# Optimization experiments

Measured on AMD Instinct MI355X. Metric: run time of the kernel, lower is better.

## Reference

```python
import jax, jax.numpy as jnp
import numpy as np
import math

B, L, D, K = 4, 2048, 1024, 3
PAD = K // 2
EPS_LN = 1e-5
EPS_NORM = 1e-12


def dwsep_conv(x_bld, dw, dwb, pw, pwb):
    # x_bld: [B, L, D] -> depthwise conv over L (groups=D) then pointwise 1x1
    x = jnp.transpose(x_bld, (0, 2, 1))  # [B, D, L]
    y = jax.lax.conv_general_dilated(
        x, dw, window_strides=(1,), padding=[(PAD, PAD)],
        feature_group_count=D, dimension_numbers=("NCH", "OIH", "NCH"))
    y = y + dwb[None, :, None]
    y = jnp.einsum("bcl,oc->bol", y, pw) + pwb[None, :, None]
    return jnp.transpose(y, (0, 2, 1))  # [B, L, D]


def l2norm(x):
    n = jnp.sqrt(jnp.sum(x * x, axis=-1, keepdims=True))
    return x / jnp.maximum(n, EPS_NORM)


def layernorm(x, g, b):
    mu = jnp.mean(x, axis=-1, keepdims=True)
    var = jnp.mean((x - mu) ** 2, axis=-1, keepdims=True)
    return (x - mu) * jax.lax.rsqrt(var + EPS_LN) * g + b


def setup_inputs() -> dict:
    key = jax.random.key(0)
    ks = jax.random.split(key, 24)
    s = 0.02
    def w(k, shape, scale=s):
        return (jax.random.normal(k, shape, dtype=jnp.float32) * scale)
    inp = {
        "x": jax.random.normal(ks[0], (B, L, D), dtype=jnp.float32),
        "wq": w(ks[1], (D, D)), "bq": jnp.zeros((D,), jnp.float32),
        "wk": w(ks[2], (D, D)), "bk": jnp.zeros((D,), jnp.float32),
        "wv": w(ks[3], (D, D)), "bv": jnp.zeros((D,), jnp.float32),
        "dwq": w(ks[4], (D, 1, K), 0.1), "dwq_b": jnp.zeros((D,), jnp.float32),
        "pwq": w(ks[5], (D, D)), "pwq_b": jnp.zeros((D,), jnp.float32),
        "dwk": w(ks[6], (D, 1, K), 0.1), "dwk_b": jnp.zeros((D,), jnp.float32),
        "pwk": w(ks[7], (D, D)), "pwk_b": jnp.zeros((D,), jnp.float32),
        "dwv": w(ks[8], (D, 1, K), 0.1), "dwv_b": jnp.zeros((D,), jnp.float32),
        "pwv": w(ks[9], (D, D)), "pwv_b": jnp.zeros((D,), jnp.float32),
        "wg": w(ks[10], (D, D)), "bg": jnp.zeros((D,), jnp.float32),
        "wo": w(ks[11], (D, D)), "bo": jnp.zeros((D,), jnp.float32),
        "mem_w": w(ks[12], (D, D)),
        "ln_g": jnp.ones((D,), jnp.float32),
        "ln_b": jnp.zeros((D,), jnp.float32),
    }
    return inp


def reference(x, wq, bq, wk, bk, wv, bv,
              dwq, dwq_b, pwq, pwq_b,
              dwk, dwk_b, pwk, pwk_b,
              dwv, dwv_b, pwv, pwv_b,
              wg, bg, wo, bo, mem_w, ln_g, ln_b):
    residual = x
    Q = jax.nn.silu(jnp.einsum("bld,ed->ble", x, wq) + bq)
    Kt = jax.nn.silu(jnp.einsum("bld,ed->ble", x, wk) + bk)
    V = jax.nn.silu(jnp.einsum("bld,ed->ble", x, wv) + bv)
    Q = dwsep_conv(Q, dwq, dwq_b, pwq, pwq_b)
    Kt = dwsep_conv(Kt, dwk, dwk_b, pwk, pwk_b)
    V = dwsep_conv(V, dwv, dwv_b, pwv, pwv_b)
    Qn = l2norm(Q)
    Kn = l2norm(Kt)
    scores = jnp.einsum("bqd,bkd->bqk", Qn, Kn) / math.sqrt(D)
    attn = jax.nn.softmax(scores, axis=-1)
    attn_out = jnp.einsum("bqk,bkd->bqd", attn, V)
    gate = jax.nn.sigmoid(jnp.einsum("bld,ed->ble", attn_out, wg) + bg)
    gated = gate * attn_out
    out = jnp.einsum("bld,ed->ble", gated, wo) + bo + residual
    out = layernorm(out, ln_g, ln_b)
    mem_pred = jnp.einsum("bld,de->ble", Kn, mem_w)
    mem_loss = jnp.mean((mem_pred - V) ** 2)
    return (out, mem_loss)
```

## Files before the change

kernel.cpp:

```cpp
#include <hip/hip_runtime.h>
#include <stdint.h>

typedef __attribute__((ext_vector_type(8))) short short8;
typedef __attribute__((ext_vector_type(4))) short short4v;
typedef __attribute__((ext_vector_type(4))) float f32x4;

#define DEV static __device__ __forceinline__

static constexpr int LL = 2048;
static constexpr int DD = 1024;
static constexpr long long BLD = 8388608LL;
static constexpr long long SLD = 2097152LL;
static constexpr long long SLLB = 4194304LL;

DEV short f2bf(float f) {
    uint32_t u = __builtin_bit_cast(uint32_t, f);
    u += 0x7fffu + ((u >> 16) & 1u);
    return (short)(u >> 16);
}
DEV float bf2f(short s) {
    uint32_t u = ((uint32_t)(uint16_t)s) << 16;
    return __builtin_bit_cast(float, u);
}

DEV float waveSum(float v) {
#pragma unroll
    for (int o = 32; o; o >>= 1) v += __shfl_down(v, o);
    return v;
}

DEV void gload16(const void* g, void* l) {
    __builtin_amdgcn_global_load_lds(
        (const __attribute__((address_space(1))) uint32_t*)(uintptr_t)g,
        (__attribute__((address_space(3))) uint32_t*)(uintptr_t)l,
        16, 0, 0);
}

__global__ __launch_bounds__(256) void k_prep(
    const float* __restrict__ x,
    const float* wq, const float* wk, const float* wv,
    const float* pq, const float* pk, const float* pv,
    const float* wg, const float* wo,
    const float* bq, const float* bk, const float* bv,
    const float* pqb, const float* pkb, const float* pvb,
    const float* __restrict__ memw,
    short* Wqkv, short* Pqkv, short* Wg, short* Wo,
    float* bqkv, float* bpw, short* MwT, short* xb, float* loss) {
    __shared__ float tile[64][65];
    const int bid = blockIdx.x;
    const int t = threadIdx.x;

    if (bid < 4096) {
        const int w = bid >> 9;
        const long long i = (long long)((bid & 511) * 256 + t) * 8;
        const float* src; short* dst;
        switch (w) {
            case 0: src = wq; dst = Wqkv;                break;
            case 1: src = wk; dst = Wqkv + 1048576;      break;
            case 2: src = wv; dst = Wqkv + 2097152;      break;
            case 3: src = pq; dst = Pqkv;                break;
            case 4: src = pk; dst = Pqkv + 1048576;      break;
            case 5: src = pv; dst = Pqkv + 2097152;      break;
            case 6: src = wg; dst = Wg;                  break;
            default: src = wo; dst = Wo;                 break;
        }
        const float4* p = (const float4*)(src + i);
        float4 a = p[0], b = p[1];
        short8 o;
        o[0] = f2bf(a.x); o[1] = f2bf(a.y); o[2] = f2bf(a.z); o[3] = f2bf(a.w);
        o[4] = f2bf(b.x); o[5] = f2bf(b.y); o[6] = f2bf(b.z); o[7] = f2bf(b.w);
        *(short8*)(dst + i) = o;
    } else if (bid < 4120) {
        const int idx = (bid - 4096) * 256 + t;
        const int sel = idx >> 10, j = idx & 1023;
        const float* s;
        switch (sel) {
            case 0: s = bq; break; case 1: s = bk; break; case 2: s = bv; break;
            case 3: s = pqb; break; case 4: s = pkb; break; default: s = pvb; break;
        }
        float v = s[j];
        if (sel < 3) bqkv[sel * 1024 + j] = v;
        else         bpw[(sel - 3) * 1024 + j] = v;
    } else if (bid < 4376) {
        const int tt = bid - 4120;
        const int r0 = (tt >> 4) * 64, c0 = (tt & 15) * 64;
#pragma unroll
        for (int i = 0; i < 16; i++) {
            int lin = i * 256 + t; int lr = lin >> 6, lc = lin & 63;
            tile[lr][lc] = memw[(long long)(r0 + lr) * DD + (c0 + lc)];
        }
        __syncthreads();
#pragma unroll
        for (int i = 0; i < 16; i++) {
            int lin = i * 256 + t; int orr = lin >> 6, oc = lin & 63;
            MwT[(long long)(c0 + orr) * DD + (r0 + oc)] = f2bf(tile[oc][orr]);
        }
    } else if (bid < 8472) {
        const long long i = (long long)((bid - 4376) * 256 + t) * 8;
        const float4* p = (const float4*)(x + i);
        float4 a = p[0], b = p[1];
        short8 o;
        o[0] = f2bf(a.x); o[1] = f2bf(a.y); o[2] = f2bf(a.z); o[3] = f2bf(a.w);
        o[4] = f2bf(b.x); o[5] = f2bf(b.y); o[6] = f2bf(b.z); o[7] = f2bf(b.w);
        *(short8*)(xb + i) = o;
    } else {
        if (t == 0) *loss = 0.f;
    }
}

__global__ __launch_bounds__(256) void k_dwconv3b(const short* __restrict__ in,
                                                  const float* __restrict__ dwq,
                                                  const float* __restrict__ dwk,
                                                  const float* __restrict__ dwv,
                                                  const float* __restrict__ dbq,
                                                  const float* __restrict__ dbk,
                                                  const float* __restrict__ dbv,
                                                  short* __restrict__ outp) {
    const int idx = blockIdx.x * 256 + threadIdx.x;
    const int d8 = idx & 127;
    const int lc = (idx >> 7) & 255;
    const int b  = (idx >> 15) & 3;
    const int br = idx >> 17;
    const float* dw = (br == 0) ? dwq : (br == 1) ? dwk : dwv;
    const float* db = (br == 0) ? dbq : (br == 1) ? dbk : dbv;

    float w[24], bb[8];
    {
        const float4* wp = (const float4*)(dw + d8 * 24);
#pragma unroll
        for (int i = 0; i < 6; i++) {
            float4 tt = wp[i];
            w[i * 4 + 0] = tt.x; w[i * 4 + 1] = tt.y;
            w[i * 4 + 2] = tt.z; w[i * 4 + 3] = tt.w;
        }
        const float4* bp = (const float4*)(db + d8 * 8);
        float4 t0 = bp[0], t1 = bp[1];
        bb[0] = t0.x; bb[1] = t0.y; bb[2] = t0.z; bb[3] = t0.w;
        bb[4] = t1.x; bb[5] = t1.y; bb[6] = t1.z; bb[7] = t1.w;
    }

    const int l0 = lc * 8;
    const long long base = ((long long)(b * LL + l0)) * 3072 + br * 1024 + d8 * 8;
    short8 xr[10];
#pragma unroll
    for (int i = 0; i < 10; i++) {
        const int l = l0 - 1 + i;
        if (l >= 0 && l < LL) xr[i] = *(const short8*)(in + base + (long long)(i - 1) * 3072);
        else { short8 z = {0, 0, 0, 0, 0, 0, 0, 0}; xr[i] = z; }
    }
#pragma unroll
    for (int j = 0; j < 8; j++) {
        short8 o;
#pragma unroll
        for (int c = 0; c < 8; c++) {
            float v = bb[c] + w[c * 3 + 0] * bf2f(xr[j][c])
                            + w[c * 3 + 1] * bf2f(xr[j + 1][c])
                            + w[c * 3 + 2] * bf2f(xr[j + 2][c]);
            o[c] = f2bf(v);
        }
        *(short8*)(outp + base + (long long)j * 3072) = o;
    }
}

__global__ __launch_bounds__(256) void k_vt_norm(const short* __restrict__ vb,
                                                 short* __restrict__ VT,
                                                 const short* __restrict__ qkb,
                                                 float* __restrict__ ninv) {
    __shared__ short tile[64][65];
    __shared__ float red[4];
    const int bid = blockIdx.x;
    const int t = threadIdx.x;
    if (bid < 2048) {
        const int z = bid >> 9, tt = bid & 511;
        const int r0 = (tt >> 4) * 64, c0 = (tt & 15) * 64;
        const short* in = vb + (long long)z * SLD;
        short* out = VT + (long long)z * SLD;
#pragma unroll
        for (int i = 0; i < 16; i++) {
            int lin = i * 256 + t; int lr = lin >> 6, lc = lin & 63;
            tile[lr][lc] = in[(long long)(r0 + lr) * 1024 + (c0 + lc)];
        }
        __syncthreads();
#pragma unroll
        for (int i = 0; i < 16; i++) {
            int lin = i * 256 + t; int orr = lin >> 6, oc = lin & 63;
            out[(long long)(c0 + orr) * 2048 + (r0 + oc)] = tile[oc][orr];
        }
    } else {
        const long long row = bid - 2048;
        const short* p = qkb + row * DD;
        short4v v = *(const short4v*)(p + t * 4);
        float f0 = bf2f(v[0]), f1 = bf2f(v[1]), f2 = bf2f(v[2]), f3 = bf2f(v[3]);
        float ss = f0 * f0 + f1 * f1 + f2 * f2 + f3 * f3;
        ss = waveSum(ss);
        if ((t & 63) == 0) red[t >> 6] = ss;
        __syncthreads();
        ss = (red[0] + red[1]) + (red[2] + red[3]);
        if (t == 0) ninv[row] = 1.f / fmaxf(sqrtf(ss), 1e-12f);
    }
}

__global__ __launch_bounds__(256) void k_rowsuminv(const short* __restrict__ sp,
                                                   float* __restrict__ rinv) {
    __shared__ float red[4];
    const long long row = blockIdx.x;
    const short* p = sp + row * 2048;
    const int t = threadIdx.x;
    short8 v = *(short8*)(p + t * 8);
    float s = 0.f;
#pragma unroll
    for (int j = 0; j < 8; j++) s += bf2f(v[j]);
    s = waveSum(s);
    if ((t & 63) == 0) red[t >> 6] = s;
    __syncthreads();
    s = (red[0] + red[1]) + (red[2] + red[3]);
    if (t == 0) rinv[row] = 1.f / s;
}

__global__ __launch_bounds__(256) void k_layernorm(float* __restrict__ y,
                                                   const float* __restrict__ g,
                                                   const float* __restrict__ b) {
    __shared__ float redS[4], redQ[4];
    const long long row = blockIdx.x;
    float* p = y + row * DD;
    const int t = threadIdx.x;
    float4 v = *(float4*)(p + t * 4);
    float s = v.x + v.y + v.z + v.w;
    float q = v.x * v.x + v.y * v.y + v.z * v.z + v.w * v.w;
    s = waveSum(s); q = waveSum(q);
    if ((t & 63) == 0) { redS[t >> 6] = s; redQ[t >> 6] = q; }
    __syncthreads();
    s = (redS[0] + redS[1]) + (redS[2] + redS[3]);
    q = (redQ[0] + redQ[1]) + (redQ[2] + redQ[3]);
    float mu = s * (1.f / DD);
    float var = q * (1.f / DD) - mu * mu;
    float rs = rsqrtf(var + 1e-5f);
    float4 o;
    o.x = (v.x - mu) * rs * g[t * 4 + 0] + b[t * 4 + 0];
    o.y = (v.y - mu) * rs * g[t * 4 + 1] + b[t * 4 + 1];
    o.z = (v.z - mu) * rs * g[t * 4 + 2] + b[t * 4 + 2];
    o.w = (v.w - mu) * rs * g[t * 4 + 3] + b[t * 4 + 3];
    *(float4*)(p + t * 4) = o;
}

enum { EPI_SILU, EPI_BIAS, EPI_EXPS, EPI_GATE, EPI_RESID };

template <int EPI>
__global__ __launch_bounds__(256, 4) void gemm(
    const short* __restrict__ A, int lda, long long sAb,
    const short* __restrict__ W, int ldw, long long sWb,
    void* __restrict__ outv, int ldo, long long sOb,
    const float* __restrict__ bias, long long sBias,
    const void* __restrict__ aux,
    int K, float scale) {
    __shared__ short lds[16384];

    const int z = blockIdx.z;
    A += (long long)z * sAb;
    W += (long long)z * sWb;

    const int tid = threadIdx.x;
    const int wid = tid >> 6, lane = tid & 63;
    const int row0 = blockIdx.y * 128, col0 = blockIdx.x * 128;
    const int wrM = (wid >> 1) * 64, wcN = (wid & 1) * 64;
    const int rl = lane & 15, kcl = lane >> 4;

    f32x4 acc[4][4] = {};

    const int srow = tid >> 3;
    const int cswz = (tid & 7) ^ (srow & 7);
    long long offA[4], offB[4];
#pragma unroll
    for (int j = 0; j < 4; j++) {
        const int rr = j * 32 + srow;
        offA[j] = (long long)(row0 + rr) * lda + cswz * 8;
        offB[j] = (long long)(col0 + rr) * ldw + cswz * 8;
    }

    const int nk = K >> 6;
    const int swz0 = (kcl ^ (rl & 7)) * 8;
    const int swz1 = ((kcl + 4) ^ (rl & 7)) * 8;

    for (int t = 0; t < nk; ++t) {
        const short* a = A + (long long)t * 64;
        const short* w = W + (long long)t * 64;
#pragma unroll
        for (int j = 0; j < 4; j++)
            gload16(a + offA[j], lds + (j * 256 + tid) * 8);
#pragma unroll
        for (int j = 0; j < 4; j++)
            gload16(w + offB[j], lds + 8192 + (j * 256 + tid) * 8);
        asm volatile("s_waitcnt vmcnt(0)" ::: "memory");
        __builtin_amdgcn_s_barrier();

        short8 af[4], bfr[4];
#pragma unroll
        for (int mi = 0; mi < 4; mi++)
            af[mi] = *(const short8*)&lds[(wrM + mi * 16 + rl) * 64 + swz0];
#pragma unroll
        for (int ni = 0; ni < 4; ni++)
            bfr[ni] = *(const short8*)&lds[8192 + (wcN + ni * 16 + rl) * 64 + swz0];
        __builtin_amdgcn_s_setprio(1);
#pragma unroll
        for (int mi = 0; mi < 4; mi++)
#pragma unroll
            for (int ni = 0; ni < 4; ni++)
                acc[mi][ni] = __builtin_amdgcn_mfma_f32_16x16x32_bf16(
                    af[mi], bfr[ni], acc[mi][ni], 0, 0, 0);
        __builtin_amdgcn_s_setprio(0);
#pragma unroll
        for (int mi = 0; mi < 4; mi++)
            af[mi] = *(const short8*)&lds[(wrM + mi * 16 + rl) * 64 + swz1];
#pragma unroll
        for (int ni = 0; ni < 4; ni++)
            bfr[ni] = *(const short8*)&lds[8192 + (wcN + ni * 16 + rl) * 64 + swz1];
        __builtin_amdgcn_s_setprio(1);
#pragma unroll
        for (int mi = 0; mi < 4; mi++)
#pragma unroll
            for (int ni = 0; ni < 4; ni++)
                acc[mi][ni] = __builtin_amdgcn_mfma_f32_16x16x32_bf16(
                    af[mi], bfr[ni], acc[mi][ni], 0, 0, 0);
        __builtin_amdgcn_s_setprio(0);
        __builtin_amdgcn_s_barrier();
    }

    const int lr4 = (lane >> 4) * 4;
    float bcol[4];
    if constexpr (EPI == EPI_SILU || EPI == EPI_BIAS || EPI == EPI_GATE || EPI == EPI_RESID) {
        const float* bz = bias + (long long)z * sBias;
#pragma unroll
        for (int ni = 0; ni < 4; ni++) bcol[ni] = bz[col0 + wcN + ni * 16 + rl];
    }
    if constexpr (EPI == EPI_EXPS) {
        const float* kz = (const float*)aux + (long long)z * 2048;
#pragma unroll
        for (int ni = 0; ni < 4; ni++) bcol[ni] = kz[col0 + wcN + ni * 16 + rl];
    }
    const float* qz = (EPI == EPI_EXPS) ? bias + (long long)z * sBias : nullptr;
#pragma unroll
    for (int mi = 0; mi < 4; mi++) {
#pragma unroll
        for (int ni = 0; ni < 4; ni++) {
            const int gc = col0 + wcN + ni * 16 + rl;
#pragma unroll
            for (int r = 0; r < 4; r++) {
                const int gr = row0 + wrM + mi * 16 + lr4 + r;
                const long long oi = (long long)gr * ldo + gc;
                float v = acc[mi][ni][r];
                if constexpr (EPI == EPI_SILU) {
                    v += bcol[ni];
                    v = v / (1.f + __expf(-v));
                    ((short*)outv + (long long)z * sOb)[oi] = f2bf(v);
                } else if constexpr (EPI == EPI_BIAS) {
                    ((short*)outv + (long long)z * sOb)[oi] = f2bf(v + bcol[ni]);
                } else if constexpr (EPI == EPI_EXPS) {
                    ((short*)outv + (long long)z * sOb)[oi] =
                        f2bf(__expf(v * qz[gr] * bcol[ni] * scale));
                } else if constexpr (EPI == EPI_GATE) {
                    float g = 1.f / (1.f + __expf(-(v + bcol[ni])));
                    float a = bf2f(((const short*)aux)[oi]);
                    ((short*)outv)[oi] = f2bf(g * a);
                } else if constexpr (EPI == EPI_RESID) {
                    ((float*)outv)[oi] = v + bcol[ni] + ((const float*)aux)[oi];
                }
            }
        }
    }
}

__global__ __launch_bounds__(256, 4) void k_avml(
    const short* __restrict__ P, const short* __restrict__ VT,
    const float* __restrict__ rinv, short* __restrict__ aob,
    const short* __restrict__ kb, const short* __restrict__ MwT,
    const short* __restrict__ vb, const float* __restrict__ kinv,
    float* __restrict__ lossOut) {
    __shared__ short lds[16384];

    const int bid = blockIdx.x;
    const bool isAV = bid < 512;
    const short* A; const short* W;
    int lda, ldw, K, row0, col0;
    const float* rp = nullptr;
    short* outp = nullptr;
    if (isAV) {
        const int z = bid >> 7, rem = bid & 127;
        row0 = (rem >> 3) * 128; col0 = (rem & 7) * 128;
        A = P + (long long)z * SLLB;  lda = 2048;
        W = VT + (long long)z * SLD;  ldw = 2048;
        K = 2048;
        outp = aob + (long long)z * SLD;
        rp = rinv + z * 2048;
    } else {
        const int rem = bid - 512;
        row0 = (rem >> 3) * 128; col0 = (rem & 7) * 128;
        A = kb; lda = 1024; W = MwT; ldw = 1024; K = 1024;
    }

    const int tid = threadIdx.x;
    const int wid = tid >> 6, lane = tid & 63;
    const int wrM = (wid >> 1) * 64, wcN = (wid & 1) * 64;
    const int rl = lane & 15, kcl = lane >> 4;

    f32x4 acc[4][4] = {};

    const int srow = tid >> 3;
    const int cswz = (tid & 7) ^ (srow & 7);
    long long offA[4], offB[4];
#pragma unroll
    for (int j = 0; j < 4; j++) {
        const int rr = j * 32 + srow;
        offA[j] = (long long)(row0 + rr) * lda + cswz * 8;
        offB[j] = (long long)(col0 + rr) * ldw + cswz * 8;
    }

    const int nk = K >> 6;
    const int swz0 = (kcl ^ (rl & 7)) * 8;
    const int swz1 = ((kcl + 4) ^ (rl & 7)) * 8;

    for (int t = 0; t < nk; ++t) {
        const short* a = A + (long long)t * 64;
        const short* w = W + (long long)t * 64;
#pragma unroll
        for (int j = 0; j < 4; j++)
            gload16(a + offA[j], lds + (j * 256 + tid) * 8);
#pragma unroll
        for (int j = 0; j < 4; j++)
            gload16(w + offB[j], lds + 8192 + (j * 256 + tid) * 8);
        asm volatile("s_waitcnt vmcnt(0)" ::: "memory");
        __builtin_amdgcn_s_barrier();

        short8 af[4], bfr[4];
#pragma unroll
        for (int mi = 0; mi < 4; mi++)
            af[mi] = *(const short8*)&lds[(wrM + mi * 16 + rl) * 64 + swz0];
#pragma unroll
        for (int ni = 0; ni < 4; ni++)
            bfr[ni] = *(const short8*)&lds[8192 + (wcN + ni * 16 + rl) * 64 + swz0];
        __builtin_amdgcn_s_setprio(1);
#pragma unroll
        for (int mi = 0; mi < 4; mi++)
#pragma unroll
            for (int ni = 0; ni < 4; ni++)
                acc[mi][ni] = __builtin_amdgcn_mfma_f32_16x16x32_bf16(
                    af[mi], bfr[ni], acc[mi][ni], 0, 0, 0);
        __builtin_amdgcn_s_setprio(0);
#pragma unroll
        for (int mi = 0; mi < 4; mi++)
            af[mi] = *(const short8*)&lds[(wrM + mi * 16 + rl) * 64 + swz1];
#pragma unroll
        for (int ni = 0; ni < 4; ni++)
            bfr[ni] = *(const short8*)&lds[8192 + (wcN + ni * 16 + rl) * 64 + swz1];
        __builtin_amdgcn_s_setprio(1);
#pragma unroll
        for (int mi = 0; mi < 4; mi++)
#pragma unroll
            for (int ni = 0; ni < 4; ni++)
                acc[mi][ni] = __builtin_amdgcn_mfma_f32_16x16x32_bf16(
                    af[mi], bfr[ni], acc[mi][ni], 0, 0, 0);
        __builtin_amdgcn_s_setprio(0);
        __builtin_amdgcn_s_barrier();
    }

    const int lr4 = (lane >> 4) * 4;
    if (isAV) {
#pragma unroll
        for (int mi = 0; mi < 4; mi++) {
#pragma unroll
            for (int ni = 0; ni < 4; ni++) {
                const int gc = col0 + wcN + ni * 16 + rl;
#pragma unroll
                for (int r = 0; r < 4; r++) {
                    const int gr = row0 + wrM + mi * 16 + lr4 + r;
                    outp[(long long)gr * 1024 + gc] = f2bf(acc[mi][ni][r] * rp[gr]);
                }
            }
        }
    } else {
        float lsum = 0.f;
#pragma unroll
        for (int mi = 0; mi < 4; mi++) {
#pragma unroll
            for (int ni = 0; ni < 4; ni++) {
                const int gc = col0 + wcN + ni * 16 + rl;
#pragma unroll
                for (int r = 0; r < 4; r++) {
                    const int gr = row0 + wrM + mi * 16 + lr4 + r;
                    float dd = acc[mi][ni][r] * kinv[gr] - bf2f(vb[(long long)gr * 1024 + gc]);
                    lsum += dd * dd;
                }
            }
        }
        lsum = waveSum(lsum);
        if (lane == 0) atomicAdd(lossOut, lsum * (1.f / (float)BLD));
    }
}


extern "C" void kernel_launch(void* const* d_in, const int* in_sizes, int n_in,
                              void* d_out, int out_size, void* d_ws, size_t ws_size,
                              hipStream_t stream) {
    const float* x    = (const float*)d_in[0];
    const float* wq   = (const float*)d_in[1];
    const float* bq   = (const float*)d_in[2];
    const float* wk   = (const float*)d_in[3];
    const float* bk   = (const float*)d_in[4];
    const float* wvw  = (const float*)d_in[5];
    const float* bvv  = (const float*)d_in[6];
    const float* dwq  = (const float*)d_in[7];
    const float* dwqb = (const float*)d_in[8];
    const float* pwq  = (const float*)d_in[9];
    const float* pwqb = (const float*)d_in[10];
    const float* dwk  = (const float*)d_in[11];
    const float* dwkb = (const float*)d_in[12];
    const float* pwk  = (const float*)d_in[13];
    const float* pwkb = (const float*)d_in[14];
    const float* dwv  = (const float*)d_in[15];
    const float* dwvb = (const float*)d_in[16];
    const float* pwv  = (const float*)d_in[17];
    const float* pwvb = (const float*)d_in[18];
    const float* wg   = (const float*)d_in[19];
    const float* bg   = (const float*)d_in[20];
    const float* wo   = (const float*)d_in[21];
    const float* bo   = (const float*)d_in[22];
    const float* memw = (const float*)d_in[23];
    const float* lng  = (const float*)d_in[24];
    const float* lnb  = (const float*)d_in[25];

    float* out = (float*)d_out;
    float* loss = out + BLD;

    char* base = (char*)d_ws;
    size_t off = 0;
    auto take = [&](size_t n) -> char* {
        char* p = base + off;
        off += (n + 255) & ~(size_t)255;
        return p;
    };
    const size_t WB = (size_t)DD * DD * 2;
    const size_t XB = (size_t)BLD * 2;
    short* Wqkv = (short*)take(3 * WB);
    short* Pqkv = (short*)take(3 * WB);
    short* Wgb  = (short*)take(WB);
    short* Wob  = (short*)take(WB);
    short* MwT  = (short*)take(WB);
    float* bqkv = (float*)take(3072 * 4);
    float* bpw  = (float*)take(3072 * 4);
    float* rinv = (float*)take(8192 * 4);
    float* ninv = (float*)take(16384 * 4);
    short* xb   = (short*)take(XB);
    short* pre  = (short*)take(3 * XB);
    short* post = (short*)take(3 * XB);

    short* qb = pre;
    short* kb = pre + BLD;
    short* vb = pre + 2 * BLD;
    short* scores = post;
    short* VT = post + 2 * BLD;
    short* aob = xb;
    short* gated = post;
    float* qinv = ninv;
    float* kinv = ninv + 8192;
    (void)ws_size; (void)in_sizes; (void)n_in; (void)out_size;

    const long long sLD = SLD;
    const long long sLLb = SLLB;

    k_prep<<<8473, 256, 0, stream>>>(
        x, wq, wk, wvw, pwq, pwk, pwv, wg, wo,
        bq, bk, bvv, pwqb, pwkb, pwvb, memw,
        Wqkv, Pqkv, Wgb, Wob, bqkv, bpw, MwT, xb, loss);

    gemm<EPI_SILU><<<dim3(24, 64, 1), 256, 0, stream>>>(
        xb, 1024, 0, Wqkv, 1024, 0, pre, 3072, 0, bqkv, 0, nullptr, 1024, 0.f);

    k_dwconv3b<<<1536, 256, 0, stream>>>(pre, dwq, dwk, dwv, dwqb, dwkb, dwvb, post);

    gemm<EPI_BIAS><<<dim3(8, 64, 3), 256, 0, stream>>>(
        post, 3072, 1024, Pqkv, 1024, (long long)DD * DD, qb, 1024, BLD,
        bpw, 1024, nullptr, 1024, 0.f);

    k_vt_norm<<<18432, 256, 0, stream>>>(vb, VT, qb, ninv);

    gemm<EPI_EXPS><<<dim3(16, 16, 4), 256, 0, stream>>>(
        qb, 1024, sLD, kb, 1024, sLD, scores, 2048, sLLb,
        qinv, 2048, kinv, 1024, 0.03125f);
    k_rowsuminv<<<8192, 256, 0, stream>>>(scores, rinv);

    k_avml<<<1024, 256, 0, stream>>>(scores, VT, rinv, aob, kb, MwT, vb, kinv, loss);

    gemm<EPI_GATE><<<dim3(8, 64, 1), 256, 0, stream>>>(
        aob, 1024, 0, Wgb, 1024, 0, gated, 1024, 0, bg, 0, aob, 1024, 0.f);

    gemm<EPI_RESID><<<dim3(8, 64, 1), 256, 0, stream>>>(
        gated, 1024, 0, Wob, 1024, 0, out, 1024, 0, bo, 0, x, 1024, 0.f);
    k_layernorm<<<8192, 256, 0, stream>>>(out, lng, lnb);
}
```

Measured before the change: 379.0 us.

## Fuse softmax row sums into score GEMM epilogue via atomics; remap AV blocks per XCD

The separate row-sum kernel over the bf16 score matrix is removed. Instead, the exp-score GEMM epilogue reduces each row's partial sums across lanes and atomically adds them into a zeroed rsum buffer, and the AV kernel divides by that sum. The AV/memory-loss block indices are also remapped so consecutive row strips land on the same XCD for better L2 reuse. This saves a full pass over the 32MB score matrix and a launch, at the cost of float atomics, which are non-deterministic. The sums now come from fp32 values rather than bf16-rounded ones.

```diff
diff --git a/kernel.cpp b/kernel.cpp
--- a/kernel.cpp
+++ b/kernel.cpp
@@ -45,7 +45,8 @@
     const float* pqb, const float* pkb, const float* pvb,
     const float* __restrict__ memw,
     short* Wqkv, short* Pqkv, short* Wg, short* Wo,
-    float* bqkv, float* bpw, short* MwT, short* xb, float* loss) {
+    float* bqkv, float* bpw, short* MwT, short* xb, float* loss,
+    float* rsum) {
     __shared__ float tile[64][65];
     const int bid = blockIdx.x;
     const int t = threadIdx.x;
@@ -103,8 +104,10 @@
         o[0] = f2bf(a.x); o[1] = f2bf(a.y); o[2] = f2bf(a.z); o[3] = f2bf(a.w);
         o[4] = f2bf(b.x); o[5] = f2bf(b.y); o[6] = f2bf(b.z); o[7] = f2bf(b.w);
         *(short8*)(xb + i) = o;
+    } else if (bid == 8472) {
+        if (t == 0) *loss = 0.f;
     } else {
-        if (t == 0) *loss = 0.f;
+        rsum[(bid - 8473) * 256 + t] = 0.f;
     }
 }
 
@@ -198,23 +201,6 @@
         ss = (red[0] + red[1]) + (red[2] + red[3]);
         if (t == 0) ninv[row] = 1.f / fmaxf(sqrtf(ss), 1e-12f);
     }
-}
-
-__global__ __launch_bounds__(256) void k_rowsuminv(const short* __restrict__ sp,
-                                                   float* __restrict__ rinv) {
-    __shared__ float red[4];
-    const long long row = blockIdx.x;
-    const short* p = sp + row * 2048;
-    const int t = threadIdx.x;
-    short8 v = *(short8*)(p + t * 8);
-    float s = 0.f;
-#pragma unroll
-    for (int j = 0; j < 8; j++) s += bf2f(v[j]);
-    s = waveSum(s);
-    if ((t & 63) == 0) red[t >> 6] = s;
-    __syncthreads();
-    s = (red[0] + red[1]) + (red[2] + red[3]);
-    if (t == 0) rinv[row] = 1.f / s;
 }
 
 __global__ __launch_bounds__(256) void k_layernorm(float* __restrict__ y,
@@ -252,7 +238,7 @@
     void* __restrict__ outv, int ldo, long long sOb,
     const float* __restrict__ bias, long long sBias,
     const void* __restrict__ aux,
-    int K, float scale) {
+    int K, float scale, float* __restrict__ rsum) {
     __shared__ short lds[16384];
 
     const int z = blockIdx.z;
@@ -326,74 +312,101 @@
     }
 
     const int lr4 = (lane >> 4) * 4;
-    float bcol[4];
-    if constexpr (EPI == EPI_SILU || EPI == EPI_BIAS || EPI == EPI_GATE || EPI == EPI_RESID) {
-        const float* bz = bias + (long long)z * sBias;
-#pragma unroll
-        for (int ni = 0; ni < 4; ni++) bcol[ni] = bz[col0 + wcN + ni * 16 + rl];
-    }
     if constexpr (EPI == EPI_EXPS) {
+        const float* qz = bias + (long long)z * sBias;
         const float* kz = (const float*)aux + (long long)z * 2048;
-#pragma unroll
-        for (int ni = 0; ni < 4; ni++) bcol[ni] = kz[col0 + wcN + ni * 16 + rl];
-    }
-    const float* qz = (EPI == EPI_EXPS) ? bias + (long long)z * sBias : nullptr;
-#pragma unroll
-    for (int mi = 0; mi < 4; mi++) {
-#pragma unroll
-        for (int ni = 0; ni < 4; ni++) {
-            const int gc = col0 + wcN + ni * 16 + rl;
-#pragma unroll
-            for (int r = 0; r < 4; r++) {
-                const int gr = row0 + wrM + mi * 16 + lr4 + r;
-                const long long oi = (long long)gr * ldo + gc;
-                float v = acc[mi][ni][r];
-                if constexpr (EPI == EPI_SILU) {
-                    v += bcol[ni];
-                    v = v / (1.f + __expf(-v));
-                    ((short*)outv + (long long)z * sOb)[oi] = f2bf(v);
-                } else if constexpr (EPI == EPI_BIAS) {
-                    ((short*)outv + (long long)z * sOb)[oi] = f2bf(v + bcol[ni]);
-                } else if constexpr (EPI == EPI_EXPS) {
-                    ((short*)outv + (long long)z * sOb)[oi] =
-                        f2bf(__expf(v * qz[gr] * bcol[ni] * scale));
-                } else if constexpr (EPI == EPI_GATE) {
-                    float g = 1.f / (1.f + __expf(-(v + bcol[ni])));
-                    float a = bf2f(((const short*)aux)[oi]);
-                    ((short*)outv)[oi] = f2bf(g * a);
-                } else if constexpr (EPI == EPI_RESID) {
-                    ((float*)outv)[oi] = v + bcol[ni] + ((const float*)aux)[oi];
+        float* rs = rsum + (long long)z * 2048;
+        short* op = (short*)outv + (long long)z * sOb;
+        float kc4[4];
+#pragma unroll
+        for (int ni = 0; ni < 4; ni++) kc4[ni] = kz[col0 + wcN + ni * 16 + rl];
+#pragma unroll
+        for (int mi = 0; mi < 4; mi++) {
+            float ps[4] = {0.f, 0.f, 0.f, 0.f};
+#pragma unroll
+            for (int ni = 0; ni < 4; ni++) {
+                const int gc = col0 + wcN + ni * 16 + rl;
+#pragma unroll
+                for (int r = 0; r < 4; r++) {
+                    const int gr = row0 + wrM + mi * 16 + lr4 + r;
+                    float p = __expf(acc[mi][ni][r] * qz[gr] * kc4[ni] * scale);
+                    op[(long long)gr * ldo + gc] = f2bf(p);
+                    ps[r] += p;
                 }
             }
+#pragma unroll
+            for (int r = 0; r < 4; r++) {
+                float v = ps[r];
+                v += __shfl_xor(v, 1);
+                v += __shfl_xor(v, 2);
+                v += __shfl_xor(v, 4);
+                v += __shfl_xor(v, 8);
+                if ((lane & 15) == 0)
+                    atomicAdd(&rs[row0 + wrM + mi * 16 + lr4 + r], v);
+            }
+        }
+    } else {
+        float bcol[4];
+        const float* bz = bias + (long long)z * sBias;
+#pragma unroll
+        for (int ni = 0; ni < 4; ni++) bcol[ni] = bz[col0 + wcN + ni * 16 + rl];
+#pragma unroll
+        for (int mi = 0; mi < 4; mi++) {
+#pragma unroll
+            for (int ni = 0; ni < 4; ni++) {
+                const int gc = col0 + wcN + ni * 16 + rl;
+#pragma unroll
+                for (int r = 0; r < 4; r++) {
+                    const int gr = row0 + wrM + mi * 16 + lr4 + r;
+                    const long long oi = (long long)gr * ldo + gc;
+                    float v = acc[mi][ni][r];
+                    if constexpr (EPI == EPI_SILU) {
+                        v += bcol[ni];
+                        v = v / (1.f + __expf(-v));
+                        ((short*)outv + (long long)z * sOb)[oi] = f2bf(v);
+                    } else if constexpr (EPI == EPI_BIAS) {
+                        ((short*)outv + (long long)z * sOb)[oi] = f2bf(v + bcol[ni]);
+                    } else if constexpr (EPI == EPI_GATE) {
+                        float g = 1.f / (1.f + __expf(-(v + bcol[ni])));
+                        float a = bf2f(((const short*)aux)[oi]);
+                        ((short*)outv)[oi] = f2bf(g * a);
+                    } else if constexpr (EPI == EPI_RESID) {
+                        ((float*)outv)[oi] = v + bcol[ni] + ((const float*)aux)[oi];
+                    }
+                }
+            }
         }
     }
 }
 
 __global__ __launch_bounds__(256, 4) void k_avml(
     const short* __restrict__ P, const short* __restrict__ VT,
-    const float* __restrict__ rinv, short* __restrict__ aob,
+    const float* __restrict__ rsum, short* __restrict__ aob,
     const short* __restrict__ kb, const short* __restrict__ MwT,
     const short* __restrict__ vb, const float* __restrict__ kinv,
     float* __restrict__ lossOut) {
     __shared__ short lds[16384];
 
     const int bid = blockIdx.x;
-    const bool isAV = bid < 512;
+    const int xcd = bid & 7, j = bid >> 3;
+    const bool isAV = j < 64;
     const short* A; const short* W;
     int lda, ldw, K, row0, col0;
     const float* rp = nullptr;
     short* outp = nullptr;
     if (isAV) {
-        const int z = bid >> 7, rem = bid & 127;
-        row0 = (rem >> 3) * 128; col0 = (rem & 7) * 128;
+        const int strip = xcd * 8 + (j >> 3);
+        const int z = strip >> 4;
+        row0 = (strip & 15) * 128; col0 = (j & 7) * 128;
         A = P + (long long)z * SLLB;  lda = 2048;
         W = VT + (long long)z * SLD;  ldw = 2048;
         K = 2048;
         outp = aob + (long long)z * SLD;
-        rp = rinv + z * 2048;
+        rp = rsum + z * 2048;
     } else {
-        const int rem = bid - 512;
-        row0 = (rem >> 3) * 128; col0 = (rem & 7) * 128;
+        const int jj = j - 64;
+        const int strip = xcd * 8 + (jj >> 3);
+        row0 = strip * 128; col0 = (jj & 7) * 128;
         A = kb; lda = 1024; W = MwT; ldw = 1024; K = 1024;
     }
 
@@ -408,10 +421,10 @@
     const int cswz = (tid & 7) ^ (srow & 7);
     long long offA[4], offB[4];
 #pragma unroll
-    for (int j = 0; j < 4; j++) {
-        const int rr = j * 32 + srow;
-        offA[j] = (long long)(row0 + rr) * lda + cswz * 8;
-        offB[j] = (long long)(col0 + rr) * ldw + cswz * 8;
+    for (int jj = 0; jj < 4; jj++) {
+        const int rr = jj * 32 + srow;
+        offA[jj] = (long long)(row0 + rr) * lda + cswz * 8;
+        offB[jj] = (long long)(col0 + rr) * ldw + cswz * 8;
     }
 
     const int nk = K >> 6;
@@ -422,11 +435,11 @@
         const short* a = A + (long long)t * 64;
         const short* w = W + (long long)t * 64;
 #pragma unroll
-        for (int j = 0; j < 4; j++)
-            gload16(a + offA[j], lds + (j * 256 + tid) * 8);
-#pragma unroll
-        for (int j = 0; j < 4; j++)
-            gload16(w + offB[j], lds + 8192 + (j * 256 + tid) * 8);
+        for (int jj = 0; jj < 4; jj++)
+            gload16(a + offA[jj], lds + (jj * 256 + tid) * 8);
+#pragma unroll
+        for (int jj = 0; jj < 4; jj++)
+            gload16(w + offB[jj], lds + 8192 + (jj * 256 + tid) * 8);
         asm volatile("s_waitcnt vmcnt(0)" ::: "memory");
         __builtin_amdgcn_s_barrier();
 
@@ -472,7 +485,7 @@
 #pragma unroll
                 for (int r = 0; r < 4; r++) {
                     const int gr = row0 + wrM + mi * 16 + lr4 + r;
-                    outp[(long long)gr * 1024 + gc] = f2bf(acc[mi][ni][r] * rp[gr]);
+                    outp[(long long)gr * 1024 + gc] = f2bf(acc[mi][ni][r] / rp[gr]);
                 }
             }
         }
@@ -546,7 +559,7 @@
     short* MwT  = (short*)take(WB);
     float* bqkv = (float*)take(3072 * 4);
     float* bpw  = (float*)take(3072 * 4);
-    float* rinv = (float*)take(8192 * 4);
+    float* rsum = (float*)take(8192 * 4);
     float* ninv = (float*)take(16384 * 4);
     short* xb   = (short*)take(XB);
     short* pre  = (short*)take(3 * XB);
@@ -566,33 +579,32 @@
     const long long sLD = SLD;
     const long long sLLb = SLLB;
 
-    k_prep<<<8473, 256, 0, stream>>>(
+    k_prep<<<8505, 256, 0, stream>>>(
         x, wq, wk, wvw, pwq, pwk, pwv, wg, wo,
         bq, bk, bvv, pwqb, pwkb, pwvb, memw,
-        Wqkv, Pqkv, Wgb, Wob, bqkv, bpw, MwT, xb, loss);
+        Wqkv, Pqkv, Wgb, Wob, bqkv, bpw, MwT, xb, loss, rsum);
 
     gemm<EPI_SILU><<<dim3(24, 64, 1), 256, 0, stream>>>(
-        xb, 1024, 0, Wqkv, 1024, 0, pre, 3072, 0, bqkv, 0, nullptr, 1024, 0.f);
+        xb, 1024, 0, Wqkv, 1024, 0, pre, 3072, 0, bqkv, 0, nullptr, 1024, 0.f, nullptr);
 
     k_dwconv3b<<<1536, 256, 0, stream>>>(pre, dwq, dwk, dwv, dwqb, dwkb, dwvb, post);
 
     gemm<EPI_BIAS><<<dim3(8, 64, 3), 256, 0, stream>>>(
         post, 3072, 1024, Pqkv, 1024, (long long)DD * DD, qb, 1024, BLD,
-        bpw, 1024, nullptr, 1024, 0.f);
+        bpw, 1024, nullptr, 1024, 0.f, nullptr);
 
     k_vt_norm<<<18432, 256, 0, stream>>>(vb, VT, qb, ninv);
 
     gemm<EPI_EXPS><<<dim3(16, 16, 4), 256, 0, stream>>>(
         qb, 1024, sLD, kb, 1024, sLD, scores, 2048, sLLb,
-        qinv, 2048, kinv, 1024, 0.03125f);
-    k_rowsuminv<<<8192, 256, 0, stream>>>(scores, rinv);
-
-    k_avml<<<1024, 256, 0, stream>>>(scores, VT, rinv, aob, kb, MwT, vb, kinv, loss);
+        qinv, 2048, kinv, 1024, 0.03125f, rsum);
+
+    k_avml<<<1024, 256, 0, stream>>>(scores, VT, rsum, aob, kb, MwT, vb, kinv, loss);
 
     gemm<EPI_GATE><<<dim3(8, 64, 1), 256, 0, stream>>>(
-        aob, 1024, 0, Wgb, 1024, 0, gated, 1024, 0, bg, 0, aob, 1024, 0.f);
+        aob, 1024, 0, Wgb, 1024, 0, gated, 1024, 0, bg, 0, aob, 1024, 0.f, nullptr);
 
     gemm<EPI_RESID><<<dim3(8, 64, 1), 256, 0, stream>>>(
-        gated, 1024, 0, Wob, 1024, 0, out, 1024, 0, bo, 0, x, 1024, 0.f);
+        gated, 1024, 0, Wob, 1024, 0, out, 1024, 0, bo, 0, x, 1024, 0.f, nullptr);
     k_layernorm<<<8192, 256, 0, stream>>>(out, lng, lnb);
 }
```

Result: faster. 345.0 us (-9.0%).
